# Kernel optimization log

Hardware: AMD Instinct MI355X
Metric: run time of the kernel (lower is better)

The kernel has to match this reference:

```python
import jax, jax.numpy as jnp
import numpy as np

NUM_EXPERTS = 8


def setup_inputs() -> dict:
    key = jax.random.key(0)
    k1, k2, k3 = jax.random.split(key, 3)
    M, K, E, N, TOPK = 16384, 1024, NUM_EXPERTS, 2048, 2
    local_hidden_states = jax.random.normal(k1, (M, K), dtype=jnp.float32)
    up_weight = jax.random.normal(k2, (E, K, N), dtype=jnp.float32) * 0.02
    full_topk_ids = jax.random.randint(k3, (M, TOPK), 0, E, dtype=jnp.int64)
    return {
        "local_hidden_states": local_hidden_states,
        "up_weight": up_weight,
        "full_topk_ids": full_topk_ids,
    }


def reference(local_hidden_states, up_weight, full_topk_ids):
    # WORLD_SIZE == 1 -> all-gather is the identity; full token set == local shard.
    full_hidden = local_hidden_states                     # [M, K]
    M, K = full_hidden.shape
    E, _, N = up_weight.shape
    topk = full_topk_ids.shape[1]

    # Each token is routed to `topk` experts: replicate rows, flatten routing ids.
    h_rep = jnp.repeat(full_hidden, topk, axis=0)         # [M*topk, K]
    flat_ids = full_topk_ids.reshape(-1)                  # [M*topk]

    # Expert-grouped GEMM: out[p] = h_rep[p] @ up_weight[flat_ids[p]].
    # Loop over the small fixed expert count, masking rows (dense reference
    # for the irregular grouped GEMM; avoids a [M*topk, K, N] weight gather).
    inter = jnp.zeros((M * topk, N), dtype=full_hidden.dtype)
    for e in range(E):
        mask = (flat_ids == e).astype(full_hidden.dtype)[:, None]   # [M*topk, 1]
        inter = inter + (h_rep @ up_weight[e]) * mask                # [M*topk, N]

    # Fused gated SiLU: split the fused gate/up projection in half.
    half = N // 2
    gate, up = inter[:, :half], inter[:, half:]
    return jax.nn.silu(gate) * up                          # [M*topk, N//2]
```

## Files before the change

### kernel.cpp

```cpp
#include <hip/hip_runtime.h>
#include <hip/hip_bf16.h>
#include <stdint.h>

typedef __attribute__((ext_vector_type(4))) float f32x4;
typedef __attribute__((ext_vector_type(8))) short bf16x8;
typedef __attribute__((ext_vector_type(4))) float float4v;

static constexpr int KD    = 1024;
static constexpr int ND    = 2048;
static constexpr int NE    = 8;
static constexpr int MROWS = 16384;
static constexpr int RFLAT = 32768;
static constexpr int OUTN  = 1024;

static constexpr size_t WS_ROWLIST = 1024;
static constexpr size_t WS_HB      = 262144;
static constexpr size_t WS_WT      = 262144 + (size_t)33554432;

__device__ __forceinline__ unsigned short f2bf(float f) {
  uint32_t u = __float_as_uint(f);
  uint32_t r = (u + 0x7FFFu + ((u >> 16) & 1u)) >> 16;
  return (unsigned short)r;
}

__device__ __forceinline__ void gload16(const void* g, void* l) {
  __builtin_amdgcn_global_load_lds(
      (__attribute__((address_space(1))) void*)(void*)g,
      (__attribute__((address_space(3))) void*)l, 16, 0, 0);
}

__global__ void k_detect(const int* __restrict__ ids32, int* __restrict__ wsi) {
  int t = blockIdx.x * 256 + threadIdx.x;
  int i = 2 * t + 1;
  if (i < RFLAT && ids32[i] != 0) atomicOr(&wsi[31], 1);
}

__device__ __forceinline__ int read_id(const int* ids32, int t, int mode) {
  return (mode ? ids32[t] : ids32[2 * t]) & 7;
}

__global__ void k_count(const int* __restrict__ ids, int* __restrict__ wsi) {
  __shared__ int h[8];
  const int tid = threadIdx.x;
  if (tid < 8) h[tid] = 0;
  __syncthreads();
  const int mode = wsi[31];
  const int base = blockIdx.x * 512 + tid;
  atomicAdd(&h[read_id(ids, base, mode)], 1);
  atomicAdd(&h[read_id(ids, base + 256, mode)], 1);
  __syncthreads();
  if (tid < 8 && h[tid]) atomicAdd(&wsi[tid], h[tid]);
}

__global__ void k_scan(int* wsi) {
  if (threadIdx.x == 0) {
    int o = 0, to = 0;
    for (int e = 0; e < NE; ++e) {
      int c = wsi[e];
      wsi[16 + e] = o;
      wsi[8 + e]  = o;
      wsi[40 + e] = to;
      o += c;
      to += (c + 127) / 128;
    }
    wsi[16 + NE] = o;
    wsi[40 + NE] = to;
  }
}

__global__ void k_scatter(const int* __restrict__ ids, int* __restrict__ wsi,
                          int* __restrict__ rowlist) {
  __shared__ int h[8], base[8], c2[8];
  const int tid = threadIdx.x;
  if (tid < 8) { h[tid] = 0; c2[tid] = 0; }
  __syncthreads();
  const int mode = wsi[31];
  const int t = blockIdx.x * 256 + tid;
  const int e = read_id(ids, t, mode);
  atomicAdd(&h[e], 1);
  __syncthreads();
  if (tid < 8 && h[tid]) base[tid] = atomicAdd(&wsi[8 + tid], h[tid]);
  __syncthreads();
  const int r = atomicAdd(&c2[e], 1);
  rowlist[base[e] + r] = t;
}

__global__ void k_cvtH(const float* __restrict__ H, unsigned short* __restrict__ Hb) {
  const int n4 = (MROWS * KD) / 4;
  const int stride = gridDim.x * blockDim.x;
  for (int i = blockIdx.x * blockDim.x + threadIdx.x; i < n4; i += stride) {
    float4v v = ((const float4v*)H)[i];
    ushort4 o;
    o.x = f2bf(v.x); o.y = f2bf(v.y); o.z = f2bf(v.z); o.w = f2bf(v.w);
    ((ushort4*)Hb)[i] = o;
  }
}

__global__ void k_cvtW(const float* __restrict__ W, unsigned short* __restrict__ Wt) {
  __shared__ float tile[64][65];
  const int e  = blockIdx.z;
  const int n0 = blockIdx.x * 64;
  const int k0 = blockIdx.y * 64;
  const int t  = threadIdx.x;
  const int tx = t & 63, ty = t >> 6;
  const float* Wp = W + (size_t)e * KD * ND;
  #pragma unroll
  for (int i = ty; i < 64; i += 8)
    tile[i][tx] = Wp[(size_t)(k0 + i) * ND + n0 + tx];
  __syncthreads();
  const int n = t >> 3, kc8 = (t & 7) * 8;
  ushort4 o0, o1;
  o0.x = f2bf(tile[kc8 + 0][n]); o0.y = f2bf(tile[kc8 + 1][n]);
  o0.z = f2bf(tile[kc8 + 2][n]); o0.w = f2bf(tile[kc8 + 3][n]);
  o1.x = f2bf(tile[kc8 + 4][n]); o1.y = f2bf(tile[kc8 + 5][n]);
  o1.z = f2bf(tile[kc8 + 6][n]); o1.w = f2bf(tile[kc8 + 7][n]);
  unsigned short* Wo = Wt + (size_t)e * ND * KD + (size_t)(n0 + n) * KD + k0 + kc8;
  *(ushort4*)Wo = o0;
  *(ushort4*)(Wo + 4) = o1;
}

__global__ __launch_bounds__(256, 3) void k_gemm(
    const unsigned short* __restrict__ Hb, const unsigned short* __restrict__ Wt,
    const int* __restrict__ wsi, const int* __restrict__ rowlist,
    float* __restrict__ Out) {
  const int bid = blockIdx.x;
  const int xcd = bid & 7;
  const int j   = bid >> 3;
  const int colblk = j & 15;
  const int rt  = xcd + (j >> 4) * 8;
  if (rt >= wsi[48]) return;
  int e = 0;
  #pragma unroll
  for (int q = 1; q < 8; ++q)
    if (rt >= wsi[40 + q]) e = q;
  const int cnt = wsi[e];
  const int tile_base = (rt - wsi[40 + e]) * 128;
  const int tile_cnt = min(128, cnt - tile_base);
  const int off = wsi[16 + e] + tile_base;
  const int c0 = colblk * 64;

  constexpr int SLOT = 16384;
  __shared__ char lds[2 * SLOT];
  __shared__ int s_rows[128];

  const int t = threadIdx.x;
  if (t < 128) s_rows[t] = rowlist[off + min(t, tile_cnt - 1)];
  __syncthreads();

  const int srow = t >> 2;
  const int coff = ((t & 3) ^ ((t >> 3) & 3)) * 16;
  const char* sA0 = (const char*)Hb + (size_t)(s_rows[srow] >> 1) * (KD * 2) + coff;
  const char* sA1 = (const char*)Hb + (size_t)(s_rows[64 + srow] >> 1) * (KD * 2) + coff;
  auto wcol_of = [&](int jc) {
    const int wn_s = jc >> 6, r64 = jc & 63;
    const int h_s = r64 >> 4, l_s = r64 & 15;
    return (h_s < 2) ? (c0 + wn_s * 32 + h_s * 16 + l_s)
                     : (OUTN + c0 + wn_s * 32 + (h_s - 2) * 16 + l_s);
  };
  const char* sB0 = (const char*)Wt + ((size_t)e * ND + wcol_of(srow)) * (KD * 2) + coff;
  const char* sB1 = (const char*)Wt + ((size_t)e * ND + wcol_of(64 + srow)) * (KD * 2) + coff;

  const int lane = t & 63, wid = t >> 6;
  const int wm = wid >> 1, wn = wid & 1;
  const int kc = lane >> 4, l15 = lane & 15;

  f32x4 acc[4][4];
  #pragma unroll
  for (int m = 0; m < 4; ++m)
    #pragma unroll
    for (int h = 0; h < 4; ++h)
      acc[m][h] = (f32x4){0.f, 0.f, 0.f, 0.f};

  int aoff[4], boff[4];
  #pragma unroll
  for (int m = 0; m < 4; ++m) {
    const int r = wm * 64 + m * 16 + l15;
    aoff[m] = r * 64 + ((kc ^ ((r >> 1) & 3)) * 16);
  }
  #pragma unroll
  for (int h = 0; h < 4; ++h) {
    const int jc = wn * 64 + h * 16 + l15;
    boff[h] = 8192 + jc * 64 + ((kc ^ ((jc >> 1) & 3)) * 16);
  }

  auto SAB = [&](int h, char* slot) {
    const int go = h * 64;
    gload16(sA0 + go, slot + t * 16);
    gload16(sA1 + go, slot + 4096 + t * 16);
    gload16(sB0 + go, slot + 8192 + t * 16);
    gload16(sB1 + go, slot + 12288 + t * 16);
  };

  bf16x8 af[4], bfv[4];
  auto LD = [&](const char* cb) {
    #pragma unroll
    for (int m = 0; m < 4; ++m) af[m] = *(const bf16x8*)(cb + aoff[m]);
    #pragma unroll
    for (int h = 0; h < 4; ++h) bfv[h] = *(const bf16x8*)(cb + boff[h]);
  };
  auto MM = [&]() {
    __builtin_amdgcn_s_setprio(1);
    #pragma unroll
    for (int m = 0; m < 4; ++m)
      #pragma unroll
      for (int h = 0; h < 4; ++h)
        acc[m][h] =
            __builtin_amdgcn_mfma_f32_16x16x32_bf16(af[m], bfv[h], acc[m][h], 0, 0, 0);
    __builtin_amdgcn_s_setprio(0);
  };
#define GUARD0 asm volatile("s_waitcnt vmcnt(0)" ::: "memory")
#define BAR __builtin_amdgcn_s_barrier()

  SAB(0, lds);
  GUARD0; BAR;

  for (int k = 0; k < 31; ++k) {
    char* cb = lds + (k & 1) * SLOT;
    char* nb = lds + ((k + 1) & 1) * SLOT;
    SAB(k + 1, nb);
    LD(cb);
    MM();
    GUARD0; BAR;
  }
  LD(lds + SLOT);
  MM();
#undef GUARD0
#undef BAR

  #pragma unroll
  for (int m = 0; m < 4; ++m) {
    const int rbase = wm * 64 + m * 16 + kc * 4;
    #pragma unroll
    for (int i = 0; i < 4; ++i) {
      const int rl = rbase + i;
      if (rl < tile_cnt) {
        const size_t orow = (size_t)s_rows[rl] * OUTN;
        #pragma unroll
        for (int h = 0; h < 2; ++h) {
          float gg = acc[m][h][i];
          float uu = acc[m][h + 2][i];
          float s = gg / (1.0f + __expf(-gg)) * uu;
          Out[orow + c0 + wn * 32 + h * 16 + l15] = s;
        }
      }
    }
  }
}

extern "C" void kernel_launch(void* const* d_in, const int* in_sizes, int n_in,
                              void* d_out, int out_size, void* d_ws, size_t ws_size,
                              hipStream_t stream) {
  const float* H  = (const float*)d_in[0];
  const float* W  = (const float*)d_in[1];
  const int* ids  = (const int*)d_in[2];
  float* Out      = (float*)d_out;
  char* ws        = (char*)d_ws;
  int* wsi        = (int*)ws;
  int* rowlist    = (int*)(ws + WS_ROWLIST);
  unsigned short* Hb = (unsigned short*)(ws + WS_HB);
  unsigned short* Wt = (unsigned short*)(ws + WS_WT);

  hipMemsetAsync(ws, 0, 1024, stream);
  k_detect<<<RFLAT / 2 / 256, 256, 0, stream>>>(ids, wsi);
  k_count<<<RFLAT / 512, 256, 0, stream>>>(ids, wsi);
  k_scan<<<1, 64, 0, stream>>>(wsi);
  k_scatter<<<RFLAT / 256, 256, 0, stream>>>(ids, wsi, rowlist);
  k_cvtH<<<2048, 256, 0, stream>>>(H, Hb);
  k_cvtW<<<dim3(ND / 64, KD / 64, NE), 512, 0, stream>>>(W, Wt);
  k_gemm<<<8 * 33 * 16, 256, 0, stream>>>(Hb, Wt, wsi, rowlist, Out);
}
```

Baseline: 228.2 us.

## Triple-buffer GEMM LDS pipeline and fold id-width detection into routing kernels

The GEMM main loop moves from a double-buffered LDS scheme to a three-slot ring with loads issued two k-steps ahead. It waits only until four loads remain outstanding instead of draining all of them, so global-load latency overlaps with more MFMA work. LDS use grows to 48KB per block, which may lower occupancy under launch_bounds(256,3). The separate k_detect launch is removed; each count/scatter block now checks the first 256 odd int32 words itself to tell int64 ids from int32 ids. That check only samples a prefix of the ids, so it could misdetect the format on unusual inputs.

```diff
diff --git a/kernel.cpp b/kernel.cpp
--- a/kernel.cpp
+++ b/kernel.cpp
@@ -29,22 +29,24 @@
       (__attribute__((address_space(3))) void*)l, 16, 0, 0);
 }
 
-__global__ void k_detect(const int* __restrict__ ids32, int* __restrict__ wsi) {
-  int t = blockIdx.x * 256 + threadIdx.x;
-  int i = 2 * t + 1;
-  if (i < RFLAT && ids32[i] != 0) atomicOr(&wsi[31], 1);
-}
-
 __device__ __forceinline__ int read_id(const int* ids32, int t, int mode) {
   return (mode ? ids32[t] : ids32[2 * t]) & 7;
 }
 
+__device__ __forceinline__ int local_mode(const int* ids, int tid, int* smode) {
+  if (tid == 0) *smode = 0;
+  __syncthreads();
+  if (tid < 256 && ids[2 * tid + 1] != 0) atomicOr(smode, 1);
+  __syncthreads();
+  return *smode;
+}
+
 __global__ void k_count(const int* __restrict__ ids, int* __restrict__ wsi) {
   __shared__ int h[8];
+  __shared__ int smode;
   const int tid = threadIdx.x;
   if (tid < 8) h[tid] = 0;
-  __syncthreads();
-  const int mode = wsi[31];
+  const int mode = local_mode(ids, tid, &smode);
   const int base = blockIdx.x * 512 + tid;
   atomicAdd(&h[read_id(ids, base, mode)], 1);
   atomicAdd(&h[read_id(ids, base + 256, mode)], 1);
@@ -71,10 +73,10 @@
 __global__ void k_scatter(const int* __restrict__ ids, int* __restrict__ wsi,
                           int* __restrict__ rowlist) {
   __shared__ int h[8], base[8], c2[8];
+  __shared__ int smode;
   const int tid = threadIdx.x;
   if (tid < 8) { h[tid] = 0; c2[tid] = 0; }
-  __syncthreads();
-  const int mode = wsi[31];
+  const int mode = local_mode(ids, tid, &smode);
   const int t = blockIdx.x * 256 + tid;
   const int e = read_id(ids, t, mode);
   atomicAdd(&h[e], 1);
@@ -140,7 +142,7 @@
   const int c0 = colblk * 64;
 
   constexpr int SLOT = 16384;
-  __shared__ char lds[2 * SLOT];
+  __shared__ char lds[3 * SLOT];
   __shared__ int s_rows[128];
 
   const int t = threadIdx.x;
@@ -208,22 +210,29 @@
             __builtin_amdgcn_mfma_f32_16x16x32_bf16(af[m], bfv[h], acc[m][h], 0, 0, 0);
     __builtin_amdgcn_s_setprio(0);
   };
+#define GUARD4 asm volatile("s_waitcnt vmcnt(4)" ::: "memory")
 #define GUARD0 asm volatile("s_waitcnt vmcnt(0)" ::: "memory")
 #define BAR __builtin_amdgcn_s_barrier()
 
   SAB(0, lds);
+  SAB(1, lds + SLOT);
+  GUARD4; BAR;
+
+  char* s0 = lds;
+  char* s1 = lds + SLOT;
+  char* s2 = lds + 2 * SLOT;
+  for (int k = 0; k < 30; ++k) {
+    SAB(k + 2, s2);
+    LD(s0);
+    MM();
+    GUARD4; BAR;
+    char* tmp = s0; s0 = s1; s1 = s2; s2 = tmp;
+  }
+  LD(s0); MM();
   GUARD0; BAR;
-
-  for (int k = 0; k < 31; ++k) {
-    char* cb = lds + (k & 1) * SLOT;
-    char* nb = lds + ((k + 1) & 1) * SLOT;
-    SAB(k + 1, nb);
-    LD(cb);
-    MM();
-    GUARD0; BAR;
-  }
-  LD(lds + SLOT);
-  MM();
+  { char* tmp = s0; s0 = s1; s1 = s2; s2 = tmp; }
+  LD(s0); MM();
+#undef GUARD4
 #undef GUARD0
 #undef BAR
 
@@ -261,7 +270,6 @@
   unsigned short* Wt = (unsigned short*)(ws + WS_WT);
 
   hipMemsetAsync(ws, 0, 1024, stream);
-  k_detect<<<RFLAT / 2 / 256, 256, 0, stream>>>(ids, wsi);
   k_count<<<RFLAT / 512, 256, 0, stream>>>(ids, wsi);
   k_scan<<<1, 64, 0, stream>>>(wsi);
   k_scatter<<<RFLAT / 256, 256, 0, stream>>>(ids, wsi, rowlist);
```

Result: faster. 222.1 us (-2.6%).
